# Kernel tuning notes

Measured on AMD Instinct MI355X. Metric: run time of the kernel, lower is better.

## Reference

```python
import jax, jax.numpy as jnp
import numpy as np

BATCH, DIM, STEPS = 64, 4096, 128


def setup_inputs() -> dict:
    key = jax.random.key(0)
    k1, = jax.random.split(key, 1)
    input_spikes = jax.random.uniform(k1, (BATCH, DIM, STEPS), dtype=jnp.float32)
    states = jnp.zeros((BATCH, DIM), dtype=jnp.float32)  # init membrane potential v
    threshold = jnp.float32(1.0)
    return {"input_spikes": input_spikes, "states": states, "threshold": threshold}


def reference(input_spikes, states, threshold):
    # Integrate-and-fire with soft reset, scanned over the trailing time axis.
    xs = jnp.moveaxis(input_spikes, -1, 0)  # [T, B, D]

    def step(v, x):
        v = v + x                                   # integrate
        fired = v >= threshold
        spike = fired.astype(v.dtype)               # hard 0/1 (constants in torch => no grad)
        v = jnp.where(fired, v - threshold, v)      # soft reset
        return v, spike

    v_final, spikes = jax.lax.scan(step, states, xs)
    return jnp.moveaxis(spikes, 0, -1), v_final  # ([B, D, T], [B, D])
```

## Files before the change

kernel.cpp:

```cpp
#include <hip/hip_runtime.h>


#define T_STEPS 128
#define TC 32
#define NCHUNK (T_STEPS / TC)
#define ROWS 256
#define LDS_STRIDE 33

__global__ __launch_bounds__(256, 4) void if_encoder_kernel(
    const float* __restrict__ x,
    const float* __restrict__ v0,
    const float* __restrict__ thr_p,
    float* __restrict__ spikes,
    float* __restrict__ vfin,
    int nrows)
{
    __shared__ float tile[ROWS * LDS_STRIDE];

    const int tid = threadIdx.x;
    const int rowbase = blockIdx.x * ROWS;
    const float thr = thr_p[0];

    const int myrow = rowbase + tid;
    float v = (myrow < nrows) ? v0[myrow] : 0.0f;

    for (int c = 0; c < NCHUNK; ++c) {
        #pragma unroll
        for (int it = 0; it < 8; ++it) {
            const int j  = it * 256 + tid;
            const int r  = j >> 3;
            const int t4 = j & 7;
            const float4 val = reinterpret_cast<const float4*>(
                x + (size_t)(rowbase + r) * T_STEPS + (size_t)c * TC)[t4];
            float* dst = &tile[r * LDS_STRIDE + t4 * 4];
            dst[0] = val.x; dst[1] = val.y; dst[2] = val.z; dst[3] = val.w;
        }
        __syncthreads();

        {
            float* row = &tile[tid * LDS_STRIDE];
            #pragma unroll
            for (int t = 0; t < TC; ++t) {
                v += row[t];
                const bool fired = (v >= thr);
                row[t] = fired ? 1.0f : 0.0f;
                v = fired ? (v - thr) : v;
            }
        }
        __syncthreads();

        #pragma unroll
        for (int it = 0; it < 8; ++it) {
            const int j  = it * 256 + tid;
            const int r  = j >> 3;
            const int t4 = j & 7;
            const float* src = &tile[r * LDS_STRIDE + t4 * 4];
            const float4 val = make_float4(src[0], src[1], src[2], src[3]);
            reinterpret_cast<float4*>(
                spikes + (size_t)(rowbase + r) * T_STEPS + (size_t)c * TC)[t4] = val;
        }
        __syncthreads();
    }

    if (myrow < nrows) vfin[myrow] = v;
}

extern "C" void kernel_launch(void* const* d_in, const int* in_sizes, int n_in,
                              void* d_out, int out_size, void* d_ws, size_t ws_size,
                              hipStream_t stream) {
    const float* x     = (const float*)d_in[0];
    const float* v0    = (const float*)d_in[1];
    const float* thr_p = (const float*)d_in[2];

    const int nrows = in_sizes[1];
    float* spikes = (float*)d_out;
    float* vfin   = (float*)d_out + (size_t)nrows * T_STEPS;

    const int blocks = (nrows + ROWS - 1) / ROWS;
    if_encoder_kernel<<<blocks, ROWS, 0, stream>>>(x, v0, thr_p, spikes, vfin, nrows);
}
```

Measured before the change: 244.4 us.

## Double-buffer chunks with direct global-to-LDS loads in single-wave blocks

Rewrites the kernel so each 64-thread block handles 64 rows. Input chunks are loaded straight into LDS with global_load_lds into two buffers, so the next chunk's load overlaps the current scan and store. An XOR swizzle replaces the padded LDS stride to avoid bank conflicts while allowing float4 LDS access. The goal is to hide global memory latency and cut register/LDS staging traffic. In exchange it relies on hand-placed vmcnt waits and launches many more small blocks. A scalar fallback handles partial tail blocks.

```diff
diff --git a/kernel.cpp b/kernel.cpp
--- a/kernel.cpp
+++ b/kernel.cpp
@@ -3,66 +3,117 @@
 
 #define T_STEPS 128
 #define TC 32
-#define NCHUNK (T_STEPS / TC)
-#define ROWS 256
-#define LDS_STRIDE 33
+#define ROWS 64
+#define BUF_F (ROWS * TC)
 
-__global__ __launch_bounds__(256, 4) void if_encoder_kernel(
-    const float* __restrict__ x,
-    const float* __restrict__ v0,
-    const float* __restrict__ thr_p,
-    float* __restrict__ spikes,
-    float* __restrict__ vfin,
-    int nrows)
+typedef unsigned int u32;
+typedef const __attribute__((address_space(1))) u32 gu32;
+typedef __attribute__((address_space(3))) u32 lu32;
+
+__device__ __forceinline__ void pf_chunk(const float* __restrict__ x, float* buf,
+                                         int rowbase, int c, int r_off, int s_ln) {
+    #pragma unroll
+    for (int k = 0; k < 8; ++k) {
+        const float* gsrc = x + (size_t)(rowbase + k * 8 + r_off) * T_STEPS
+                              + c * TC + s_ln * 4;
+        __builtin_amdgcn_global_load_lds((gu32*)gsrc, (lu32*)(buf + k * 256), 16, 0, 0);
+    }
+}
+
+__device__ __forceinline__ float scan_chunk(float* buf, int lane, float v, float thr) {
+    float* base = buf + lane * TC;
+    const int rx = lane & 7;
+    #pragma unroll
+    for (int s4 = 0; s4 < 8; ++s4) {
+        float4* p = reinterpret_cast<float4*>(base + ((s4 ^ rx) << 2));
+        const float4 xv = *p;
+        float4 sp;
+        v += xv.x; { const bool f = v >= thr; sp.x = f ? 1.0f : 0.0f; v = f ? v - thr : v; }
+        v += xv.y; { const bool f = v >= thr; sp.y = f ? 1.0f : 0.0f; v = f ? v - thr : v; }
+        v += xv.z; { const bool f = v >= thr; sp.z = f ? 1.0f : 0.0f; v = f ? v - thr : v; }
+        v += xv.w; { const bool f = v >= thr; sp.w = f ? 1.0f : 0.0f; v = f ? v - thr : v; }
+        *p = sp;
+    }
+    return v;
+}
+
+__device__ __forceinline__ void st_chunk(float* __restrict__ spikes, const float* buf,
+                                         int rowbase, int c, int lane, int r_off, int s_ln) {
+    #pragma unroll
+    for (int k = 0; k < 8; ++k) {
+        const float4 d = *reinterpret_cast<const float4*>(buf + (k * 64 + lane) * 4);
+        *reinterpret_cast<float4*>(spikes + (size_t)(rowbase + k * 8 + r_off) * T_STEPS
+                                   + c * TC + s_ln * 4) = d;
+    }
+}
+
+#define WAIT_VM(n) asm volatile("s_waitcnt vmcnt(" #n ")" ::: "memory")
+#define WAIT_LGKM0 asm volatile("s_waitcnt lgkmcnt(0)" ::: "memory")
+
+__global__ __launch_bounds__(64) void if_encoder_kernel(
+    const float* __restrict__ x, const float* __restrict__ v0,
+    const float* __restrict__ thr_p, float* __restrict__ spikes,
+    float* __restrict__ vfin, int nrows)
 {
-    __shared__ float tile[ROWS * LDS_STRIDE];
+    __shared__ __align__(16) float lds[2 * BUF_F];
+    float* buf0 = lds;
+    float* buf1 = lds + BUF_F;
 
-    const int tid = threadIdx.x;
+    const int lane = threadIdx.x;
     const int rowbase = blockIdx.x * ROWS;
-    const float thr = thr_p[0];
+    const int r_off = lane >> 3;
+    const int s_ln  = (lane & 7) ^ r_off;
 
-    const int myrow = rowbase + tid;
-    float v = (myrow < nrows) ? v0[myrow] : 0.0f;
+    if (rowbase + ROWS <= nrows) {
+        float v = v0[rowbase + lane];
+        const float thr = thr_p[0];
 
-    for (int c = 0; c < NCHUNK; ++c) {
-        #pragma unroll
-        for (int it = 0; it < 8; ++it) {
-            const int j  = it * 256 + tid;
-            const int r  = j >> 3;
-            const int t4 = j & 7;
-            const float4 val = reinterpret_cast<const float4*>(
-                x + (size_t)(rowbase + r) * T_STEPS + (size_t)c * TC)[t4];
-            float* dst = &tile[r * LDS_STRIDE + t4 * 4];
-            dst[0] = val.x; dst[1] = val.y; dst[2] = val.z; dst[3] = val.w;
+        pf_chunk(x, buf0, rowbase, 0, r_off, s_ln);
+        pf_chunk(x, buf1, rowbase, 1, r_off, s_ln);
+
+        WAIT_VM(8);
+        v = scan_chunk(buf0, lane, v, thr);
+        __syncthreads();
+        st_chunk(spikes, buf0, rowbase, 0, lane, r_off, s_ln);
+        WAIT_LGKM0;
+        __builtin_amdgcn_sched_barrier(0);
+        pf_chunk(x, buf0, rowbase, 2, r_off, s_ln);
+
+        WAIT_VM(16);
+        v = scan_chunk(buf1, lane, v, thr);
+        __syncthreads();
+        st_chunk(spikes, buf1, rowbase, 1, lane, r_off, s_ln);
+        WAIT_LGKM0;
+        __builtin_amdgcn_sched_barrier(0);
+        pf_chunk(x, buf1, rowbase, 3, r_off, s_ln);
+
+        WAIT_VM(16);
+        v = scan_chunk(buf0, lane, v, thr);
+        __syncthreads();
+        st_chunk(spikes, buf0, rowbase, 2, lane, r_off, s_ln);
+
+        WAIT_VM(8);
+        v = scan_chunk(buf1, lane, v, thr);
+        __syncthreads();
+        st_chunk(spikes, buf1, rowbase, 3, lane, r_off, s_ln);
+
+        vfin[rowbase + lane] = v;
+    } else {
+        const int myrow = rowbase + lane;
+        if (myrow < nrows) {
+            float v = v0[myrow];
+            const float thr = thr_p[0];
+            const float* xr = x + (size_t)myrow * T_STEPS;
+            float* sr = spikes + (size_t)myrow * T_STEPS;
+            for (int t = 0; t < T_STEPS; ++t) {
+                v += xr[t];
+                const bool f = v >= thr;
+                sr[t] = f ? 1.0f : 0.0f;
+                v = f ? v - thr : v;
+            }
+            vfin[myrow] = v;
         }
-        __syncthreads();
-
-        {
-            float* row = &tile[tid * LDS_STRIDE];
-            #pragma unroll
-            for (int t = 0; t < TC; ++t) {
-                v += row[t];
-                const bool fired = (v >= thr);
-                row[t] = fired ? 1.0f : 0.0f;
-                v = fired ? (v - thr) : v;
-            }
-        }
-        __syncthreads();
-
-        #pragma unroll
-        for (int it = 0; it < 8; ++it) {
-            const int j  = it * 256 + tid;
-            const int r  = j >> 3;
-            const int t4 = j & 7;
-            const float* src = &tile[r * LDS_STRIDE + t4 * 4];
-            const float4 val = make_float4(src[0], src[1], src[2], src[3]);
-            reinterpret_cast<float4*>(
-                spikes + (size_t)(rowbase + r) * T_STEPS + (size_t)c * TC)[t4] = val;
-        }
-        __syncthreads();
     }
-
-    if (myrow < nrows) vfin[myrow] = v;
 }
 
 extern "C" void kernel_launch(void* const* d_in, const int* in_sizes, int n_in,
```

Measured after the change: 244.6 us. Within noise of the previous version (+0.1%).

## Replace LDS-transposed tiles with per-thread register double-buffered row scan

Applied to the files above, without the earlier changes.

Removes the shared-memory tile and barriers; each thread now loads its own row with float4 loads into a two-stage register buffer and writes spikes directly. This removes LDS traffic and the synchronisation between load, compute and store phases. In exchange, global accesses become strided across a wavefront (rows 512 bytes apart), losing coalescing, and register pressure rises.

```diff
diff --git a/kernel.cpp b/kernel.cpp
--- a/kernel.cpp
+++ b/kernel.cpp
@@ -2,12 +2,8 @@
 
 
 #define T_STEPS 128
-#define TC 32
-#define NCHUNK (T_STEPS / TC)
-#define ROWS 256
-#define LDS_STRIDE 33
 
-__global__ __launch_bounds__(256, 4) void if_encoder_kernel(
+__global__ __launch_bounds__(256) void if_scan_regs_kernel(
     const float* __restrict__ x,
     const float* __restrict__ v0,
     const float* __restrict__ thr_p,
@@ -15,54 +11,43 @@
     float* __restrict__ vfin,
     int nrows)
 {
-    __shared__ float tile[ROWS * LDS_STRIDE];
+    const int row = blockIdx.x * 256 + threadIdx.x;
+    if (row >= nrows) return;
 
-    const int tid = threadIdx.x;
-    const int rowbase = blockIdx.x * ROWS;
+    const float4* __restrict__ xr = reinterpret_cast<const float4*>(
+        x + (size_t)row * T_STEPS);
+    float4* __restrict__ sr = reinterpret_cast<float4*>(
+        spikes + (size_t)row * T_STEPS);
+
+    float4 buf[2][8];
+
+    #pragma unroll
+    for (int k = 0; k < 8; ++k) buf[0][k] = xr[k];
+
+    float v = v0[row];
     const float thr = thr_p[0];
 
-    const int myrow = rowbase + tid;
-    float v = (myrow < nrows) ? v0[myrow] : 0.0f;
-
-    for (int c = 0; c < NCHUNK; ++c) {
+    #pragma unroll
+    for (int c = 0; c < 4; ++c) {
+        const int cur = c & 1;
+        const int nxt = cur ^ 1;
+        if (c < 3) {
+            #pragma unroll
+            for (int k = 0; k < 8; ++k) buf[nxt][k] = xr[(c + 1) * 8 + k];
+        }
         #pragma unroll
-        for (int it = 0; it < 8; ++it) {
-            const int j  = it * 256 + tid;
-            const int r  = j >> 3;
-            const int t4 = j & 7;
-            const float4 val = reinterpret_cast<const float4*>(
-                x + (size_t)(rowbase + r) * T_STEPS + (size_t)c * TC)[t4];
-            float* dst = &tile[r * LDS_STRIDE + t4 * 4];
-            dst[0] = val.x; dst[1] = val.y; dst[2] = val.z; dst[3] = val.w;
+        for (int k = 0; k < 8; ++k) {
+            const float4 xv = buf[cur][k];
+            float4 sp;
+            v += xv.x; { const bool f = v >= thr; sp.x = f ? 1.0f : 0.0f; v = f ? v - thr : v; }
+            v += xv.y; { const bool f = v >= thr; sp.y = f ? 1.0f : 0.0f; v = f ? v - thr : v; }
+            v += xv.z; { const bool f = v >= thr; sp.z = f ? 1.0f : 0.0f; v = f ? v - thr : v; }
+            v += xv.w; { const bool f = v >= thr; sp.w = f ? 1.0f : 0.0f; v = f ? v - thr : v; }
+            sr[c * 8 + k] = sp;
         }
-        __syncthreads();
-
-        {
-            float* row = &tile[tid * LDS_STRIDE];
-            #pragma unroll
-            for (int t = 0; t < TC; ++t) {
-                v += row[t];
-                const bool fired = (v >= thr);
-                row[t] = fired ? 1.0f : 0.0f;
-                v = fired ? (v - thr) : v;
-            }
-        }
-        __syncthreads();
-
-        #pragma unroll
-        for (int it = 0; it < 8; ++it) {
-            const int j  = it * 256 + tid;
-            const int r  = j >> 3;
-            const int t4 = j & 7;
-            const float* src = &tile[r * LDS_STRIDE + t4 * 4];
-            const float4 val = make_float4(src[0], src[1], src[2], src[3]);
-            reinterpret_cast<float4*>(
-                spikes + (size_t)(rowbase + r) * T_STEPS + (size_t)c * TC)[t4] = val;
-        }
-        __syncthreads();
     }
 
-    if (myrow < nrows) vfin[myrow] = v;
+    vfin[row] = v;
 }
 
 extern "C" void kernel_launch(void* const* d_in, const int* in_sizes, int n_in,
@@ -76,6 +61,6 @@
     float* spikes = (float*)d_out;
     float* vfin   = (float*)d_out + (size_t)nrows * T_STEPS;
 
-    const int blocks = (nrows + ROWS - 1) / ROWS;
-    if_encoder_kernel<<<blocks, ROWS, 0, stream>>>(x, v0, thr_p, spikes, vfin, nrows);
+    const int blocks = (nrows + 255) / 256;
+    if_scan_regs_kernel<<<blocks, 256, 0, stream>>>(x, v0, thr_p, spikes, vfin, nrows);
 }
```

After: 280.3 us. 14.7% more time.
